# Kernel tuning notes

Hardware: AMD Instinct MI355X
Metric: run time of the kernel (lower is better)

Reference implementation:

```python
import jax, jax.numpy as jnp
import numpy as np

B, N, H = 16, 1024, 4
CH = (64, 128, 256, 512)
KV = 960
EPS = 1e-5  # InstanceNorm2d default eps


def setup_inputs() -> dict:
    key = jax.random.key(0)
    ks = jax.random.split(key, 16)
    s = 0.02
    inp = {
        "emb1": jax.random.normal(ks[0], (B, N, CH[0]), jnp.float32),
        "emb2": jax.random.normal(ks[1], (B, N, CH[1]), jnp.float32),
        "emb3": jax.random.normal(ks[2], (B, N, CH[2]), jnp.float32),
        "emb4": jax.random.normal(ks[3], (B, N, CH[3]), jnp.float32),
        "emb_all": jax.random.normal(ks[4], (B, N, KV), jnp.float32),
        # per-head query weights (torch Linear weight layout [out, in])
        "Wq1": jax.random.normal(ks[5], (H, CH[0] // 4, CH[0] // 4), jnp.float32) * s,
        "Wq2": jax.random.normal(ks[6], (H, CH[1] // 4, CH[1] // 4), jnp.float32) * s,
        "Wq3": jax.random.normal(ks[7], (H, CH[2] // 4, CH[2] // 4), jnp.float32) * s,
        "Wq4": jax.random.normal(ks[8], (H, CH[3] // 4, CH[3] // 4), jnp.float32) * s,
        # NOTE: original forward only ever uses self.key[0] / self.value[0]
        "Wk": jax.random.normal(ks[9], (KV // 4, KV // 4), jnp.float32) * s,
        "Wv": jax.random.normal(ks[10], (KV // 4, KV // 4), jnp.float32) * s,
        "Wo1": jax.random.normal(ks[11], (CH[0], CH[0]), jnp.float32) * s,
        "Wo2": jax.random.normal(ks[12], (CH[1], CH[1]), jnp.float32) * s,
        "Wo3": jax.random.normal(ks[13], (CH[2], CH[2]), jnp.float32) * s,
        "Wo4": jax.random.normal(ks[14], (CH[3], CH[3]), jnp.float32) * s,
    }
    return inp


def _heads_from_all(x):
    # Reproduce the per-head channel regrouping of emb_all:
    # head h takes [16h:16(h+1)] of scale1, [32h:...] of scale2, etc. -> [B,H,N,240]
    b, n, _ = x.shape
    parts = [
        x[:, :, 0:64].reshape(b, n, H, 16),
        x[:, :, 64:192].reshape(b, n, H, 32),
        x[:, :, 192:448].reshape(b, n, H, 64),
        x[:, :, 448:960].reshape(b, n, H, 128),
    ]
    return jnp.concatenate(parts, axis=-1).transpose(0, 2, 1, 3)


def _scale_attn(emb, Wq, Wo, Kh, Vh):
    b, n, c = emb.shape
    d = c // H
    q = emb.reshape(b, n, H, d)
    # per-head linear (torch: x @ W.T): [B,H,N,d]
    Qh = jnp.einsum('bnhd,hed->bhne', q, Wq)
    # channel attention: Q^T K -> [B,H,d,240]
    scores = jnp.einsum('bhnd,bhnk->bhdk', Qh, Kh) / np.float32(np.sqrt(KV))
    # InstanceNorm2d over heads (per (b,h), normalize over last two dims, biased var)
    m = scores.mean(axis=(2, 3), keepdims=True)
    v = scores.var(axis=(2, 3), keepdims=True)
    probs = jax.nn.softmax((scores - m) / jnp.sqrt(v + EPS), axis=-1)
    # probs @ V^T -> [B,H,d,N]
    ctx = jnp.einsum('bhdk,bhnk->bhdn', probs, Vh)
    # permute(0,3,2,1) -> [B,N,d,H], flatten -> [B,N,c]
    ctx = ctx.transpose(0, 3, 2, 1).reshape(b, n, c)
    return jnp.einsum('bnc,ec->bne', ctx, Wo)


def reference(emb1, emb2, emb3, emb4, emb_all,
              Wq1, Wq2, Wq3, Wq4, Wk, Wv, Wo1, Wo2, Wo3, Wo4):
    heads = _heads_from_all(emb_all)  # [B,H,N,240]
    Kh = jnp.einsum('bhnd,ed->bhne', heads, Wk)
    Vh = jnp.einsum('bhnd,ed->bhne', heads, Wv)
    O1 = _scale_attn(emb1, Wq1, Wo1, Kh, Vh)
    O2 = _scale_attn(emb2, Wq2, Wo2, Kh, Vh)
    O3 = _scale_attn(emb3, Wq3, Wo3, Kh, Vh)
    O4 = _scale_attn(emb4, Wq4, Wo4, Kh, Vh)
    return (O1, O2, O3, O4)
```

## Files before the change

kernel.cpp:

```cpp
#include <hip/hip_runtime.h>
#include <hip/hip_bf16.h>
#include <math.h>

#define B_   16
#define N_   1024
#define H_   4
#define D240 240
#define SC_  57600

typedef unsigned short ushort;
typedef __attribute__((ext_vector_type(8))) short bf16x8;
typedef __attribute__((ext_vector_type(4))) float f32x4;

__device__ __forceinline__ ushort f2b(float v) {
  __hip_bfloat16 h = __float2bfloat16(v);
  return *reinterpret_cast<ushort*>(&h);
}

__device__ __forceinline__ void gload16(const void* g, void* s) {
  __builtin_amdgcn_global_load_lds((const __attribute__((address_space(1))) void*)g,
                                   (__attribute__((address_space(3))) void*)s, 16, 0, 0);
}

__global__ __launch_bounds__(256) void conv_inputs(const float* __restrict__ emb_all,
                                                   const float* __restrict__ e1,
                                                   const float* __restrict__ e2,
                                                   const float* __restrict__ e3,
                                                   const float* __restrict__ e4,
                                                   ushort* __restrict__ heads,
                                                   ushort* __restrict__ embh) {
  const int bn = blockIdx.x;
  const int b = bn >> 10, n = bn & 1023;
  const float* ha = emb_all + (long)bn * 960;

  for (int u = threadIdx.x; u < 512; u += 256) {
    const int slot = u * 2;
    const int h = slot >> 8, k = slot & 255;
    long dsti = (((long)b * H_ + h) * N_ + n) * 256 + k;
    float hv0 = 0.f, hv1 = 0.f;
    if (k < 16)       { const float* p = ha + h * 16 + k;              hv0 = p[0]; hv1 = p[1]; }
    else if (k < 48)  { const float* p = ha + 64 + h * 32 + (k - 16);  hv0 = p[0]; hv1 = p[1]; }
    else if (k < 112) { const float* p = ha + 192 + h * 64 + (k - 48); hv0 = p[0]; hv1 = p[1]; }
    else if (k < 240) { const float* p = ha + 448 + h * 128 + (k - 112); hv0 = p[0]; hv1 = p[1]; }
    ushort2 hw; hw.x = f2b(hv0); hw.y = f2b(hv1);
    *(ushort2*)(heads + dsti) = hw;
    float ev0 = 0.f, ev1 = 0.f;
    if (k < 16)       { const float* p = e1 + (long)bn * 64  + h * 16  + k;         ev0 = p[0]; ev1 = p[1]; }
    else if (k < 48)  { const float* p = e2 + (long)bn * 128 + h * 32  + (k - 16);  ev0 = p[0]; ev1 = p[1]; }
    else if (k < 112) { const float* p = e3 + (long)bn * 256 + h * 64  + (k - 48);  ev0 = p[0]; ev1 = p[1]; }
    else if (k < 240) { const float* p = e4 + (long)bn * 512 + h * 128 + (k - 112); ev0 = p[0]; ev1 = p[1]; }
    ushort2 ew; ew.x = f2b(ev0); ew.y = f2b(ev1);
    *(ushort2*)(embh + dsti) = ew;
  }
}

__global__ __launch_bounds__(256) void conv_weights(
    const float* __restrict__ Wk, const float* __restrict__ Wv,
    const float* __restrict__ q1, const float* __restrict__ q2,
    const float* __restrict__ q3, const float* __restrict__ q4,
    const float* __restrict__ o1, const float* __restrict__ o2,
    const float* __restrict__ o3, const float* __restrict__ o4,
    ushort* __restrict__ wts) {
  long i = (long)blockIdx.x * 256 + threadIdx.x;
  if (i >= 716800) return;
  float v = 0.f;
  if (i < 122880) {
    const float* src = (i < 61440) ? Wk : Wv;
    long j = (i < 61440) ? i : i - 61440;
    int r = j / 256, k = j % 256;
    if (k < 240) v = src[(long)r * 240 + k];
  } else if (i < 368640) {
    long j = i - 122880;
    int h = j / 61440; int rem = j % 61440;
    int r = rem / 256, k = rem % 256;
    int s = r < 16 ? 0 : r < 48 ? 1 : r < 112 ? 2 : 3;
    const int dss[4] = {16, 32, 64, 128};
    const int qf[4]  = {0, 16, 48, 112};
    const float* qs[4] = {q1, q2, q3, q4};
    int d = dss[s], off = qf[s];
    if (k >= off && k < off + d)
      v = qs[s][((long)(h * d + (r - off))) * d + (k - off)];
  } else {
    long j = i - 368640;
    int s = j < 4096 ? 0 : j < 20480 ? 1 : j < 86016 ? 2 : 3;
    const long base[4] = {0, 4096, 20480, 86016};
    const int cs[4] = {64, 128, 256, 512};
    const float* os[4] = {o1, o2, o3, o4};
    long rem = j - base[s];
    int c = cs[s], d = c >> 2;
    int e = rem / c, kk = rem % c;
    v = os[s][(long)e * c + (kk % d) * 4 + kk / d];
  }
  wts[i] = f2b(v);
}

__global__ __launch_bounds__(256) void mfma_abT(
    const ushort* __restrict__ A, long lda, long AsY, long AsZ,
    const ushort* __restrict__ Bm, long ldb, long BsY, long BsZ,
    void* __restrict__ Cv, long ldc, long CsY, long CsZ,
    int M, int Nn, int Npad, int K, float alpha, int c_bf16, int tilesN)
{
  A  += blockIdx.y * AsY + blockIdx.z * AsZ;
  Bm += blockIdx.y * BsY + blockIdx.z * BsZ;

  const int m0 = (blockIdx.x / tilesN) * 128;
  const int n0 = (blockIdx.x % tilesN) * 128;
  const int tid = threadIdx.x;
  const int l = tid & 63, w = tid >> 6;
  const int wy = w >> 1, wx = w & 1;

  __shared__ __align__(16) ushort As[128 * 32];
  __shared__ __align__(16) ushort Bs[128 * 32];

  f32x4 acc[4][4];
  #pragma unroll
  for (int i = 0; i < 4; ++i)
    #pragma unroll
    for (int j = 0; j < 4; ++j) acc[i][j] = (f32x4)0.f;

  const int srow = tid >> 2;
  const int skc  = (tid & 3) * 8;
  int ra0 = m0 + srow;      ra0 = ra0 < M  ? ra0 : M - 1;
  int ra1 = m0 + srow + 64; ra1 = ra1 < M  ? ra1 : M - 1;
  int rb0 = n0 + srow;      rb0 = rb0 < Nn ? rb0 : Nn - 1;
  int rb1 = n0 + srow + 64; rb1 = rb1 < Nn ? rb1 : Nn - 1;
  const ushort* a0 = A  + (long)ra0 * lda + skc;
  const ushort* a1 = A  + (long)ra1 * lda + skc;
  const ushort* b0 = Bm + (long)rb0 * ldb + skc;
  const ushort* b1 = Bm + (long)rb1 * ldb + skc;
  ushort* lA0 = As + srow * 32 + skc;
  ushort* lA1 = As + (srow + 64) * 32 + skc;
  ushort* lB0 = Bs + srow * 32 + skc;
  ushort* lB1 = Bs + (srow + 64) * 32 + skc;

  const ushort* arp = As + (wy * 64 + (l & 15)) * 32 + (l >> 4) * 8;
  const ushort* brp = Bs + (wx * 64 + (l & 15)) * 32 + (l >> 4) * 8;

  for (int k0 = 0; k0 < K; k0 += 32) {
    __syncthreads();
    gload16(a0 + k0, lA0);
    gload16(a1 + k0, lA1);
    gload16(b0 + k0, lB0);
    gload16(b1 + k0, lB1);
    __syncthreads();
    bf16x8 af[4], bfr[4];
    #pragma unroll
    for (int i = 0; i < 4; ++i) af[i]  = *(const bf16x8*)(arp + i * 512);
    #pragma unroll
    for (int j = 0; j < 4; ++j) bfr[j] = *(const bf16x8*)(brp + j * 512);
    #pragma unroll
    for (int i = 0; i < 4; ++i)
      #pragma unroll
      for (int j = 0; j < 4; ++j)
        acc[i][j] = __builtin_amdgcn_mfma_f32_16x16x32_bf16(af[i], bfr[j], acc[i][j], 0, 0, 0);
  }

  const int quad = l >> 4, lc = l & 15;
  if (c_bf16) {
    ushort* C = (ushort*)Cv + blockIdx.y * CsY + blockIdx.z * CsZ;
    #pragma unroll
    for (int i = 0; i < 4; ++i) {
      #pragma unroll
      for (int r = 0; r < 4; ++r) {
        int row = m0 + wy * 64 + i * 16 + quad * 4 + r;
        if (row >= M) continue;
        ushort* Cr = C + (long)row * ldc;
        #pragma unroll
        for (int j = 0; j < 4; ++j) {
          int col = n0 + wx * 64 + j * 16 + lc;
          if (col < Nn) Cr[col] = f2b(acc[i][j][r] * alpha);
          else if (col < Npad) Cr[col] = 0;
        }
      }
    }
  } else {
    float* C = (float*)Cv + blockIdx.y * CsY + blockIdx.z * CsZ;
    #pragma unroll
    for (int i = 0; i < 4; ++i) {
      #pragma unroll
      for (int r = 0; r < 4; ++r) {
        int row = m0 + wy * 64 + i * 16 + quad * 4 + r;
        if (row >= M) continue;
        float* Cr = C + (long)row * ldc;
        #pragma unroll
        for (int j = 0; j < 4; ++j) {
          int col = n0 + wx * 64 + j * 16 + lc;
          if (col < Nn) Cr[col] = acc[i][j][r] * alpha;
        }
      }
    }
  }
}

__global__ __launch_bounds__(256) void mfma_ctx(const ushort* __restrict__ V,
                                                const ushort* __restrict__ P,
                                                ushort* __restrict__ ctx2) {
  const int h = blockIdx.y, b = blockIdx.z;
  const ushort* A  = V + (((long)b * H_ + h) * 1024) * 256;
  const ushort* Bm = P + (((long)b * H_ + h) * 240) * 256;

  const int m0 = (blockIdx.x >> 1) * 128;
  const int n0 = (blockIdx.x & 1) * 128;
  const int tid = threadIdx.x;
  const int l = tid & 63, w = tid >> 6;
  const int wy = w >> 1, wx = w & 1;

  __shared__ __align__(16) ushort As[128 * 32];
  __shared__ __align__(16) ushort Bs[128 * 32];

  f32x4 acc[4][4];
  #pragma unroll
  for (int i = 0; i < 4; ++i)
    #pragma unroll
    for (int j = 0; j < 4; ++j) acc[i][j] = (f32x4)0.f;

  const int srow = tid >> 2;
  const int skc  = (tid & 3) * 8;
  int rb0 = n0 + srow;      rb0 = rb0 < 240 ? rb0 : 239;
  int rb1 = n0 + srow + 64; rb1 = rb1 < 240 ? rb1 : 239;
  const ushort* a0 = A  + (long)(m0 + srow) * 256 + skc;
  const ushort* a1 = A  + (long)(m0 + srow + 64) * 256 + skc;
  const ushort* b0 = Bm + (long)rb0 * 256 + skc;
  const ushort* b1 = Bm + (long)rb1 * 256 + skc;
  ushort* lA0 = As + srow * 32 + skc;
  ushort* lA1 = As + (srow + 64) * 32 + skc;
  ushort* lB0 = Bs + srow * 32 + skc;
  ushort* lB1 = Bs + (srow + 64) * 32 + skc;

  const ushort* arp = As + (wy * 64 + (l & 15)) * 32 + (l >> 4) * 8;
  const ushort* brp = Bs + (wx * 64 + (l & 15)) * 32 + (l >> 4) * 8;

  for (int k0 = 0; k0 < 256; k0 += 32) {
    __syncthreads();
    gload16(a0 + k0, lA0);
    gload16(a1 + k0, lA1);
    gload16(b0 + k0, lB0);
    gload16(b1 + k0, lB1);
    __syncthreads();
    bf16x8 af[4], bfr[4];
    #pragma unroll
    for (int i = 0; i < 4; ++i) af[i]  = *(const bf16x8*)(arp + i * 512);
    #pragma unroll
    for (int j = 0; j < 4; ++j) bfr[j] = *(const bf16x8*)(brp + j * 512);
    #pragma unroll
    for (int i = 0; i < 4; ++i)
      #pragma unroll
      for (int j = 0; j < 4; ++j)
        acc[i][j] = __builtin_amdgcn_mfma_f32_16x16x32_bf16(af[i], bfr[j], acc[i][j], 0, 0, 0);
  }

  const int quad = l >> 4, lc = l & 15;
  const int dss[4] = {16, 32, 64, 128};
  const int qf[4]  = {0, 16, 48, 112};
  const int cf[4]  = {0, 64, 192, 448};
  #pragma unroll
  for (int i = 0; i < 4; ++i) {
    #pragma unroll
    for (int r = 0; r < 4; ++r) {
      int row = m0 + wy * 64 + i * 16 + quad * 4 + r;
      ushort* Cr = ctx2 + ((long)b * N_ + row) * 960;
      #pragma unroll
      for (int j = 0; j < 4; ++j) {
        int col = n0 + wx * 64 + j * 16 + lc;
        if (col < 240) {
          int s = col < 16 ? 0 : col < 48 ? 1 : col < 112 ? 2 : 3;
          int chan = cf[s] + h * dss[s] + (col - qf[s]);
          Cr[chan] = f2b(acc[i][j][r]);
        }
      }
    }
  }
}

__global__ __launch_bounds__(256) void in_stats(const float* __restrict__ sc,
                                                float* __restrict__ stats) {
  const int doffs[4] = {0, 16, 48, 112};
  const int dss[4]   = {16, 32, 64, 128};
  const int bh = blockIdx.x, sidx = blockIdx.y;
  const float4* S4 = (const float4*)(sc + (long)bh * SC_ + doffs[sidx] * D240);
  const int n4 = dss[sidx] * 60;

  float s = 0.f, s2 = 0.f;
  for (int i = threadIdx.x; i < n4; i += 256) {
    float4 v = S4[i];
    s  += v.x + v.y + v.z + v.w;
    s2 += v.x * v.x + v.y * v.y + v.z * v.z + v.w * v.w;
  }
  #pragma unroll
  for (int o = 32; o > 0; o >>= 1) { s += __shfl_down(s, o); s2 += __shfl_down(s2, o); }

  __shared__ float wsum[4], wsum2[4];
  const int wave = threadIdx.x >> 6, lane = threadIdx.x & 63;
  if (lane == 0) { wsum[wave] = s; wsum2[wave] = s2; }
  __syncthreads();
  if (threadIdx.x == 0) {
    float n = (float)(n4 * 4);
    float ts = wsum[0] + wsum[1] + wsum[2] + wsum[3];
    float ts2 = wsum2[0] + wsum2[1] + wsum2[2] + wsum2[3];
    float mean = ts / n;
    float var = ts2 / n - mean * mean;
    stats[(bh * 4 + sidx) * 2]     = mean;
    stats[(bh * 4 + sidx) * 2 + 1] = rsqrtf(var + 1e-5f);
  }
}

__global__ __launch_bounds__(256) void sm_apply(const float* __restrict__ sc,
                                                const float* __restrict__ stats,
                                                ushort* __restrict__ P) {
  const int bh = blockIdx.y;
  const int row = blockIdx.x * 4 + (threadIdx.x >> 6);
  const int lane = threadIdx.x & 63;
  const int s = row < 16 ? 0 : row < 48 ? 1 : row < 112 ? 2 : 3;
  const float mean = stats[(bh * 4 + s) * 2];
  const float rstd = stats[(bh * 4 + s) * 2 + 1];
  const float* r = sc + (long)bh * SC_ + (long)row * D240;
  ushort* p = P + ((long)bh * D240 + row) * 256;

  float v[4];
  float mx = -1e30f;
  #pragma unroll
  for (int j = 0; j < 4; ++j) {
    int c = lane + j * 64;
    v[j] = (c < D240) ? (r[c] - mean) * rstd : -1e30f;
    mx = fmaxf(mx, v[j]);
  }
  #pragma unroll
  for (int o = 32; o > 0; o >>= 1) mx = fmaxf(mx, __shfl_xor(mx, o));
  float sum = 0.f;
  #pragma unroll
  for (int j = 0; j < 4; ++j) {
    int c = lane + j * 64;
    v[j] = (c < D240) ? __expf(v[j] - mx) : 0.f;
    sum += v[j];
  }
  #pragma unroll
  for (int o = 32; o > 0; o >>= 1) sum += __shfl_xor(sum, o);
  float inv = 1.f / sum;
  #pragma unroll
  for (int j = 0; j < 4; ++j) {
    int c = lane + j * 64;
    p[c] = (c < D240) ? f2b(v[j] * inv) : (ushort)0;
  }
}

extern "C" void kernel_launch(void* const* d_in, const int* in_sizes, int n_in,
                              void* d_out, int out_size, void* d_ws, size_t ws_size,
                              hipStream_t stream) {
  const float* emb[4] = {(const float*)d_in[0], (const float*)d_in[1],
                         (const float*)d_in[2], (const float*)d_in[3]};
  const float* emb_all = (const float*)d_in[4];
  const float* Wq[4] = {(const float*)d_in[5], (const float*)d_in[6],
                        (const float*)d_in[7], (const float*)d_in[8]};
  const float* Wk = (const float*)d_in[9];
  const float* Wv = (const float*)d_in[10];
  const float* Wo[4] = {(const float*)d_in[11], (const float*)d_in[12],
                        (const float*)d_in[13], (const float*)d_in[14]};
  float* out = (float*)d_out;
  float* sc  = (float*)d_out;

  ushort* wsb     = (ushort*)d_ws;
  ushort* heads_b = wsb;
  ushort* ctx2    = wsb;
  ushort* emb_h   = wsb + 16777216;
  ushort* P_b     = wsb + 16777216;
  ushort* Q_T     = wsb + 33554432;
  ushort* Kh_T    = wsb + 49283072;
  ushort* Vh      = wsb + 65011712;
  ushort* wts     = wsb + 81788928;
  ushort* Wk_b  = wts;
  ushort* Wv_b  = wts + 61440;
  ushort* Wq_bd = wts + 122880;
  ushort* Wo_b  = wts + 368640;
  float*  stats = (float*)(wsb + 82505728);

  const long sbh256 = 1024L * 256;
  const int  wo[4]   = {0, 4096, 20480, 86016};
  const long ooff[4] = {0, 1048576, 3145728, 7340032};
  const int  cs[4]   = {64, 128, 256, 512};
  const float alpha_s = 1.0f / sqrtf(960.0f);

  conv_inputs<<<dim3(B_ * N_), 256, 0, stream>>>(emb_all, emb[0], emb[1], emb[2], emb[3],
                                                 heads_b, emb_h);
  conv_weights<<<dim3(2800), 256, 0, stream>>>(Wk, Wv, Wq[0], Wq[1], Wq[2], Wq[3],
                                               Wo[0], Wo[1], Wo[2], Wo[3], wts);

  mfma_abT<<<dim3(16, 64, 1), 256, 0, stream>>>(
      Wk_b, 256, 0, 0,
      heads_b, 256, sbh256, 0,
      Kh_T, 1024, 240L * 1024, 0,
      240, 1024, 1024, 256, 1.f, 1, 8);

  mfma_abT<<<dim3(16, 64, 1), 256, 0, stream>>>(
      heads_b, 256, sbh256, 0,
      Wv_b, 256, 0, 0,
      Vh, 256, sbh256, 0,
      1024, 240, 256, 256, 1.f, 1, 2);

  mfma_abT<<<dim3(16, H_, B_), 256, 0, stream>>>(
      Wq_bd, 256, 240L * 256, 0,
      emb_h, 256, sbh256, (long)H_ * sbh256,
      Q_T, 1024, 240L * 1024, 4L * 240 * 1024,
      240, 1024, 1024, 256, 1.f, 1, 8);

  mfma_abT<<<dim3(4, 64, 1), 256, 0, stream>>>(
      Q_T, 1024, 240L * 1024, 0,
      Kh_T, 1024, 240L * 1024, 0,
      sc, 240, (long)SC_, 0,
      240, 240, 240, 1024, alpha_s, 0, 2);

  in_stats<<<dim3(64, 4), 256, 0, stream>>>(sc, stats);
  sm_apply<<<dim3(60, 64), 256, 0, stream>>>(sc, stats, P_b);

  mfma_ctx<<<dim3(16, H_, B_), 256, 0, stream>>>(Vh, P_b, ctx2);

  const int coff[4] = {0, 64, 192, 448};
  for (int i = 0; i < 4; ++i) {
    int c = cs[i];
    int tn = (c + 127) / 128;
    mfma_abT<<<dim3(128 * tn, 1, 1), 256, 0, stream>>>(
        ctx2 + coff[i], 960, 0, 0,
        Wo_b + wo[i], c, 0, 0,
        out + ooff[i], c, 0, 0,
        B_ * N_, c, c, c, 1.f, 0, tn);
  }
}
```

Baseline: 418.5 us.

## Merge four output-projection GEMMs into one launch and vectorize input conversion

Result: faster. 367.1 us (-12.3%).

```diff
diff --git a/kernel.cpp b/kernel.cpp
--- a/kernel.cpp
+++ b/kernel.cpp
@@ -10,6 +10,7 @@
 
 typedef unsigned short ushort;
 typedef __attribute__((ext_vector_type(8))) short bf16x8;
+typedef __attribute__((ext_vector_type(8))) unsigned short u16x8;
 typedef __attribute__((ext_vector_type(4))) float f32x4;
 
 __device__ __forceinline__ ushort f2b(float v) {
@@ -31,27 +32,36 @@
                                                    ushort* __restrict__ embh) {
   const int bn = blockIdx.x;
   const int b = bn >> 10, n = bn & 1023;
-  const float* ha = emb_all + (long)bn * 960;
-
-  for (int u = threadIdx.x; u < 512; u += 256) {
-    const int slot = u * 2;
-    const int h = slot >> 8, k = slot & 255;
-    long dsti = (((long)b * H_ + h) * N_ + n) * 256 + k;
-    float hv0 = 0.f, hv1 = 0.f;
-    if (k < 16)       { const float* p = ha + h * 16 + k;              hv0 = p[0]; hv1 = p[1]; }
-    else if (k < 48)  { const float* p = ha + 64 + h * 32 + (k - 16);  hv0 = p[0]; hv1 = p[1]; }
-    else if (k < 112) { const float* p = ha + 192 + h * 64 + (k - 48); hv0 = p[0]; hv1 = p[1]; }
-    else if (k < 240) { const float* p = ha + 448 + h * 128 + (k - 112); hv0 = p[0]; hv1 = p[1]; }
-    ushort2 hw; hw.x = f2b(hv0); hw.y = f2b(hv1);
-    *(ushort2*)(heads + dsti) = hw;
-    float ev0 = 0.f, ev1 = 0.f;
-    if (k < 16)       { const float* p = e1 + (long)bn * 64  + h * 16  + k;         ev0 = p[0]; ev1 = p[1]; }
-    else if (k < 48)  { const float* p = e2 + (long)bn * 128 + h * 32  + (k - 16);  ev0 = p[0]; ev1 = p[1]; }
-    else if (k < 112) { const float* p = e3 + (long)bn * 256 + h * 64  + (k - 48);  ev0 = p[0]; ev1 = p[1]; }
-    else if (k < 240) { const float* p = e4 + (long)bn * 512 + h * 128 + (k - 112); ev0 = p[0]; ev1 = p[1]; }
-    ushort2 ew; ew.x = f2b(ev0); ew.y = f2b(ev1);
-    *(ushort2*)(embh + dsti) = ew;
-  }
+  const int t = threadIdx.x;
+  const int which = t >> 7;
+  const int gg = t & 127;
+  const int h = gg >> 5;
+  const int k0 = (gg & 31) * 8;
+
+  ushort* dst = (which ? embh : heads) + (((long)b * H_ + h) * N_ + n) * 256 + k0;
+
+  float4 p0 = {0.f, 0.f, 0.f, 0.f}, p1 = {0.f, 0.f, 0.f, 0.f};
+  if (k0 < 240) {
+    const float* src;
+    if (which == 0) {
+      const float* ha = emb_all + (long)bn * 960;
+      if (k0 < 16)       src = ha + h * 16 + k0;
+      else if (k0 < 48)  src = ha + 64  + h * 32  + (k0 - 16);
+      else if (k0 < 112) src = ha + 192 + h * 64  + (k0 - 48);
+      else               src = ha + 448 + h * 128 + (k0 - 112);
+    } else {
+      if (k0 < 16)       src = e1 + (long)bn * 64  + h * 16  + k0;
+      else if (k0 < 48)  src = e2 + (long)bn * 128 + h * 32  + (k0 - 16);
+      else if (k0 < 112) src = e3 + (long)bn * 256 + h * 64  + (k0 - 48);
+      else               src = e4 + (long)bn * 512 + h * 128 + (k0 - 112);
+    }
+    p0 = *(const float4*)src;
+    p1 = *(const float4*)(src + 4);
+  }
+  u16x8 w;
+  w[0] = f2b(p0.x); w[1] = f2b(p0.y); w[2] = f2b(p0.z); w[3] = f2b(p0.w);
+  w[4] = f2b(p1.x); w[5] = f2b(p1.y); w[6] = f2b(p1.z); w[7] = f2b(p1.w);
+  *(u16x8*)dst = w;
 }
 
 __global__ __launch_bounds__(256) void conv_weights(
@@ -272,6 +282,91 @@
   }
 }
 
+__global__ __launch_bounds__(256) void mfma_oproj(const ushort* __restrict__ ctx2,
+                                                  const ushort* __restrict__ Wo_b,
+                                                  float* __restrict__ out) {
+  const int bx = blockIdx.x;
+  int s = bx < 128 ? 0 : bx < 256 ? 1 : bx < 512 ? 2 : 3;
+  const int sbase[4] = {0, 128, 256, 512};
+  const int cs_[4]   = {64, 128, 256, 512};
+  const int coff_[4] = {0, 64, 192, 448};
+  const int wo_[4]   = {0, 4096, 20480, 86016};
+  const long oo_[4]  = {0, 1048576, 3145728, 7340032};
+  const int c = cs_[s];
+  const int nt = (c + 127) >> 7;
+  const int local = bx - sbase[s];
+  const int m0 = (local / nt) * 128;
+  const int n0 = (local % nt) * 128;
+
+  const ushort* A  = ctx2 + coff_[s];
+  const ushort* Bm = Wo_b + wo_[s];
+  float* C = out + oo_[s];
+  const int K = c, Nn = c;
+
+  const int tid = threadIdx.x;
+  const int l = tid & 63, w = tid >> 6;
+  const int wy = w >> 1, wx = w & 1;
+
+  __shared__ __align__(16) ushort As[128 * 32];
+  __shared__ __align__(16) ushort Bs[128 * 32];
+
+  f32x4 acc[4][4];
+  #pragma unroll
+  for (int i = 0; i < 4; ++i)
+    #pragma unroll
+    for (int j = 0; j < 4; ++j) acc[i][j] = (f32x4)0.f;
+
+  const int srow = tid >> 2;
+  const int skc  = (tid & 3) * 8;
+  int rb0 = n0 + srow;      rb0 = rb0 < Nn ? rb0 : Nn - 1;
+  int rb1 = n0 + srow + 64; rb1 = rb1 < Nn ? rb1 : Nn - 1;
+  const ushort* a0 = A  + (long)(m0 + srow) * 960 + skc;
+  const ushort* a1 = A  + (long)(m0 + srow + 64) * 960 + skc;
+  const ushort* b0 = Bm + (long)rb0 * c + skc;
+  const ushort* b1 = Bm + (long)rb1 * c + skc;
+  ushort* lA0 = As + srow * 32 + skc;
+  ushort* lA1 = As + (srow + 64) * 32 + skc;
+  ushort* lB0 = Bs + srow * 32 + skc;
+  ushort* lB1 = Bs + (srow + 64) * 32 + skc;
+
+  const ushort* arp = As + (wy * 64 + (l & 15)) * 32 + (l >> 4) * 8;
+  const ushort* brp = Bs + (wx * 64 + (l & 15)) * 32 + (l >> 4) * 8;
+
+  for (int k0 = 0; k0 < K; k0 += 32) {
+    __syncthreads();
+    gload16(a0 + k0, lA0);
+    gload16(a1 + k0, lA1);
+    gload16(b0 + k0, lB0);
+    gload16(b1 + k0, lB1);
+    __syncthreads();
+    bf16x8 af[4], bfr[4];
+    #pragma unroll
+    for (int i = 0; i < 4; ++i) af[i]  = *(const bf16x8*)(arp + i * 512);
+    #pragma unroll
+    for (int j = 0; j < 4; ++j) bfr[j] = *(const bf16x8*)(brp + j * 512);
+    #pragma unroll
+    for (int i = 0; i < 4; ++i)
+      #pragma unroll
+      for (int j = 0; j < 4; ++j)
+        acc[i][j] = __builtin_amdgcn_mfma_f32_16x16x32_bf16(af[i], bfr[j], acc[i][j], 0, 0, 0);
+  }
+
+  const int quad = l >> 4, lc = l & 15;
+  #pragma unroll
+  for (int i = 0; i < 4; ++i) {
+    #pragma unroll
+    for (int r = 0; r < 4; ++r) {
+      int row = m0 + wy * 64 + i * 16 + quad * 4 + r;
+      float* Cr = C + (long)row * c;
+      #pragma unroll
+      for (int j = 0; j < 4; ++j) {
+        int col = n0 + wx * 64 + j * 16 + lc;
+        if (col < Nn) Cr[col] = acc[i][j][r];
+      }
+    }
+  }
+}
+
 __global__ __launch_bounds__(256) void in_stats(const float* __restrict__ sc,
                                                 float* __restrict__ stats) {
   const int doffs[4] = {0, 16, 48, 112};
@@ -374,9 +469,6 @@
   float*  stats = (float*)(wsb + 82505728);
 
   const long sbh256 = 1024L * 256;
-  const int  wo[4]   = {0, 4096, 20480, 86016};
-  const long ooff[4] = {0, 1048576, 3145728, 7340032};
-  const int  cs[4]   = {64, 128, 256, 512};
   const float alpha_s = 1.0f / sqrtf(960.0f);
 
   conv_inputs<<<dim3(B_ * N_), 256, 0, stream>>>(emb_all, emb[0], emb[1], emb[2], emb[3],
@@ -413,14 +505,5 @@
 
   mfma_ctx<<<dim3(16, H_, B_), 256, 0, stream>>>(Vh, P_b, ctx2);
 
-  const int coff[4] = {0, 64, 192, 448};
-  for (int i = 0; i < 4; ++i) {
-    int c = cs[i];
-    int tn = (c + 127) / 128;
-    mfma_abT<<<dim3(128 * tn, 1, 1), 256, 0, stream>>>(
-        ctx2 + coff[i], 960, 0, 0,
-        Wo_b + wo[i], c, 0, 0,
-        out + ooff[i], c, 0, 0,
-        B_ * N_, c, c, c, 1.f, 0, tn);
-  }
-}
+  mfma_oproj<<<dim3(1024), 256, 0, stream>>>(ctx2, Wo_b, out);
+}
```
